# Optimization experiments

Hardware: AMD Instinct MI355X
Metric: run time of the kernel (lower is better)

Reference implementation:

```python
import jax, jax.numpy as jnp
import numpy as np

B, N, S, K, K2, C = 8, 131072, 1024, 64, 64, 32
RADIUS, RADIUS_POST = 0.4, 0.8
D1 = C + 6        # 38: mlp1 input (xyz + dim_box + feats)
H = 2 * C         # 64
D2 = H + 6        # 70: mlp2 input
H3 = 4 * H        # 256: mlp3 hidden


def _bgather(x, idx):
    # per-batch gather along axis 1 (points axis): x [B,N,...], idx [B,M] -> [B,M,...]
    return jax.vmap(lambda a, i: a[i])(x, idx)


def _conv_bn(x, w, s, t, relu=True):
    # 1x1 conv (matmul over channel) + folded eval-mode BN (scale/shift per channel)
    y = jnp.einsum('...c,cd->...d', x, w) * s + t
    return jnp.maximum(y, 0.0) if relu else y


def setup_inputs():
    key = jax.random.key(0)
    ks = jax.random.split(key, 20)
    inp = {
        'locs': jax.random.normal(ks[0], (B, N, 3), jnp.float32),
        'feats': jax.random.normal(ks[1], (B, C, N), jnp.float32),
        'boxes': jax.random.normal(ks[2], (B, N, 6), jnp.float32),
        'fps_inds': jax.random.randint(ks[3], (B, S), 0, N),
        'neighbor_inds': jax.random.randint(ks[4], (B, S * K), 0, N),
        'neighbor_inds2': jax.random.randint(ks[5], (B, S * K2), 0, S),
    }
    def w(k, i, o):
        return jax.random.normal(k, (i, o), jnp.float32) * (1.0 / np.sqrt(i))
    def bn(k, c):
        k1, k2 = jax.random.split(k)
        return (1.0 + 0.1 * jax.random.normal(k1, (c,), jnp.float32),
                0.1 * jax.random.normal(k2, (c,), jnp.float32))
    inp['w1a'] = w(ks[6], D1, C);  inp['s1a'], inp['t1a'] = bn(ks[7], C)
    inp['w1b'] = w(ks[8], C, H);   inp['s1b'], inp['t1b'] = bn(ks[9], H)
    inp['w2'] = w(ks[10], D2, H);  inp['s2'], inp['t2'] = bn(ks[11], H)
    inp['w3a'] = w(ks[12], H, H3); inp['s3a'], inp['t3a'] = bn(ks[13], H3)
    inp['w3b'] = w(ks[14], H3, H); inp['s3b'], inp['t3b'] = bn(ks[15], H)
    return inp


def reference(locs, feats, boxes, fps_inds, neighbor_inds, neighbor_inds2,
              w1a, s1a, t1a, w1b, s1b, t1b, w2, s2, t2,
              w3a, s3a, t3a, w3b, s3b, t3b):
    feats_nc = jnp.transpose(feats, (0, 2, 1))          # [B,N,C]
    dim_boxes = boxes[..., 3:] - boxes[..., :3]          # [B,N,3]

    fps_locs = _bgather(locs, fps_inds)                  # [B,S,3]
    fps_dim = _bgather(dim_boxes, fps_inds)              # [B,S,3]
    fps_boxes = _bgather(boxes, fps_inds)                # [B,S,6]

    # --- stage 1: ball-query gather on raw points ---
    gxyz = _bgather(locs, neighbor_inds).reshape(B, S, K, 3)
    gxyz = (gxyz - fps_locs[:, :, None, :]) / RADIUS
    gdim = _bgather(dim_boxes, neighbor_inds).reshape(B, S, K, 3)
    gdim = jnp.abs(gdim - fps_dim[:, :, None, :])
    gfeat = _bgather(feats_nc, neighbor_inds).reshape(B, S, K, C)
    g = jnp.concatenate([gxyz, gdim, gfeat], axis=-1)    # [B,S,K,38]

    h = _conv_bn(g, w1a, s1a, t1a, relu=True)
    h = _conv_bn(h, w1b, s1b, t1b, relu=True)            # [B,S,K,64]
    new_features = jnp.max(h, axis=2)                    # [B,S,64]
    identity = new_features

    # --- stage 2: ball-query gather on FPS points ---
    gxyz2 = _bgather(fps_locs, neighbor_inds2).reshape(B, S, K2, 3)
    gxyz2 = (gxyz2 - fps_locs[:, :, None, :]) / RADIUS_POST
    gdim2 = _bgather(fps_dim, neighbor_inds2).reshape(B, S, K2, 3)
    gdim2 = jnp.abs(gdim2 - fps_dim[:, :, None, :])
    gfeat2 = _bgather(new_features, neighbor_inds2).reshape(B, S, K2, H)
    g2 = jnp.concatenate([gxyz2, gdim2, gfeat2], axis=-1)  # [B,S,K2,70]

    h2 = _conv_bn(g2, w2, s2, t2, relu=False)            # [B,S,K2,64]
    h2 = jnp.max(h2, axis=2)                             # [B,S,64]

    # --- mlp_module3 (Conv1d bottleneck) + skip ---
    h3 = _conv_bn(h2, w3a, s3a, t3a, relu=True)          # [B,S,256]
    h3 = _conv_bn(h3, w3b, s3b, t3b, relu=False)         # [B,S,64]
    out = jnp.maximum(h3 + identity, 0.0)                # skip_act

    return fps_locs, jnp.transpose(out, (0, 2, 1)), fps_boxes, fps_inds
```

## Files before the change

### kernel.cpp

```cpp
#include <hip/hip_runtime.h>
#include <hip/hip_bf16.h>
#include <stdint.h>

#define DEV __device__ __forceinline__

constexpr int B_ = 8, N_ = 131072, S_ = 1024, C_ = 32;
constexpr float INV_R1 = 2.5f;
constexpr float INV_R2 = 1.25f;

constexpr int OW1AS = 0;
constexpr int OW1BS = 1216;
constexpr int OT1B  = 3264;
constexpr int OW2S  = 3328;
constexpr int OT2   = 7808;
constexpr int OW3AS = 7872;
constexpr int OT3A  = 24256;
constexpr int OW3BS = 24512;
constexpr int OT3B  = 40896;

constexpr size_t WS_CTR  = 163840;
constexpr size_t WS_NF   = WS_CTR  + (size_t)8192*104*4;
constexpr size_t WS_P2   = WS_NF   + (size_t)524288*4;
constexpr size_t WS_HOUT = WS_P2   + (size_t)524288*4;
constexpr size_t WS_PREC = WS_HOUT + (size_t)524288*4;

DEV float bfu(uint16_t u){ return __uint_as_float(((uint32_t)u) << 16); }

__global__ void k_weights(
    const float* __restrict__ w1a, const float* __restrict__ s1a,
    const float* __restrict__ w1b, const float* __restrict__ s1b,
    const float* __restrict__ t1b,
    const float* __restrict__ w2,  const float* __restrict__ s2,
    const float* __restrict__ t2,
    const float* __restrict__ w3a, const float* __restrict__ s3a,
    const float* __restrict__ t3a,
    const float* __restrict__ w3b, const float* __restrict__ s3b,
    const float* __restrict__ t3b,
    float* __restrict__ wsw)
{
  int t = blockIdx.x*256 + threadIdx.x;
  int nth = gridDim.x*256;
  for (int i=t;i<38*32;i+=nth)  wsw[OW1AS+i] = w1a[i]*s1a[i&31];
  for (int i=t;i<32*64;i+=nth)  wsw[OW1BS+i] = w1b[i]*s1b[i&63];
  for (int i=t;i<64;i+=nth)     wsw[OT1B+i]  = t1b[i];
  for (int i=t;i<70*64;i+=nth)  wsw[OW2S+i]  = w2[i]*s2[i&63];
  for (int i=t;i<64;i+=nth)     wsw[OT2+i]   = t2[i];
  for (int i=t;i<64*256;i+=nth) wsw[OW3AS+i] = w3a[i]*s3a[i&255];
  for (int i=t;i<256;i+=nth)    wsw[OT3A+i]  = t3a[i];
  for (int i=t;i<256*64;i+=nth) wsw[OW3BS+i] = w3b[i]*s3b[i&63];
  for (int i=t;i<64;i+=nth)     wsw[OT3B+i]  = t3b[i];
}

__global__ __launch_bounds__(256) void k_points(
    const float* __restrict__ locs,
    const float* __restrict__ feats,
    const float* __restrict__ wsw,
    __hip_bfloat16* __restrict__ prec)
{
  size_t p = (size_t)blockIdx.x*256 + threadIdx.x;
  int b = (int)(p >> 17);
  int pinb = (int)(p & (size_t)(N_-1));

  float x = locs[p*3+0]*INV_R1;
  float y = locs[p*3+1]*INV_R1;
  float z = locs[p*3+2]*INV_R1;

  float acc[32];
  #pragma unroll
  for (int j=0;j<32;j++)
    acc[j] = x*wsw[OW1AS+j] + y*wsw[OW1AS+32+j] + z*wsw[OW1AS+64+j];

  const float* fb = feats + (size_t)b*C_*N_ + pinb;
  float fcur[8], fnxt[8];
  #pragma unroll
  for (int i=0;i<8;i++) fcur[i] = fb[(size_t)i*N_];
  #pragma unroll
  for (int ch=0;ch<4;ch++){
    if (ch<3){
      #pragma unroll
      for (int i=0;i<8;i++) fnxt[i] = fb[(size_t)(8*(ch+1)+i)*N_];
    }
    #pragma unroll
    for (int i=0;i<8;i++){
      int c = 8*ch+i;
      #pragma unroll
      for (int j=0;j<32;j++)
        acc[j] = fmaf(fcur[i], wsw[OW1AS + (6+c)*32 + j], acc[j]);
    }
    #pragma unroll
    for (int i=0;i<8;i++) fcur[i] = fnxt[i];
  }
  union U { float4 v[4]; __hip_bfloat16 h[32]; } r;
  #pragma unroll
  for (int j=0;j<32;j++) r.h[j] = __float2bfloat16(acc[j]);
  float4* dst = (float4*)(prec + p*32);
  dst[0]=r.v[0]; dst[1]=r.v[1]; dst[2]=r.v[2]; dst[3]=r.v[3];
}

__global__ __launch_bounds__(256) void k_centers(
    const float* __restrict__ locs,
    const float* __restrict__ boxes,
    const int* __restrict__ fps_inds,
    const float* __restrict__ t1a,
    const float* __restrict__ wsw,
    float* __restrict__ ctr,
    float* __restrict__ out0,
    float* __restrict__ out2,
    float* __restrict__ out3)
{
  int i = blockIdx.x*256 + threadIdx.x;
  int b = i >> 10;
  int idx = fps_inds[i];
  size_t src = (size_t)b*N_ + (uint32_t)idx;

  float x = locs[src*3+0], y = locs[src*3+1], z = locs[src*3+2];
  out0[(size_t)i*3+0]=x; out0[(size_t)i*3+1]=y; out0[(size_t)i*3+2]=z;
  float bx0=boxes[src*6+0], bx1=boxes[src*6+1], bx2=boxes[src*6+2];
  float bx3=boxes[src*6+3], bx4=boxes[src*6+4], bx5=boxes[src*6+5];
  out2[(size_t)i*6+0]=bx0; out2[(size_t)i*6+1]=bx1; out2[(size_t)i*6+2]=bx2;
  out2[(size_t)i*6+3]=bx3; out2[(size_t)i*6+4]=bx4; out2[(size_t)i*6+5]=bx5;
  out3[i] = (float)idx;

  float d0=bx3-bx0, d1=bx4-bx1, d2=bx5-bx2;
  float* cr = ctr + (size_t)i*104;
  cr[0]=x; cr[1]=y; cr[2]=z; cr[3]=d0; cr[4]=d1; cr[5]=d2; cr[6]=0.f; cr[7]=0.f;
  float xr=x*INV_R1, yr=y*INV_R1, zr=z*INV_R1;
  #pragma unroll
  for (int j=0;j<32;j++)
    cr[8+j] = t1a[j] - xr*wsw[OW1AS+j] - yr*wsw[OW1AS+32+j] - zr*wsw[OW1AS+64+j];
  float xq=x*INV_R2, yq=y*INV_R2, zq=z*INV_R2;
  #pragma unroll
  for (int j=0;j<64;j++)
    cr[40+j] = wsw[OT2+j] - xq*wsw[OW2S+j] - yq*wsw[OW2S+64+j] - zq*wsw[OW2S+128+j];
}

__global__ __launch_bounds__(256) void k_stage1(
    const float* __restrict__ boxes,
    const int* __restrict__ neighbor_inds,
    const __hip_bfloat16* __restrict__ prec,
    const float* __restrict__ wsw,
    const float* __restrict__ ctr,
    float* __restrict__ nf,
    float* __restrict__ p2)
{
  int wid  = (blockIdx.x*256 + threadIdx.x) >> 6;
  int lane = threadIdx.x & 63;
  int uwid = __builtin_amdgcn_readfirstlane(wid);
  int b = uwid >> 10;

  int nbr = neighbor_inds[(size_t)uwid*64 + lane];
  size_t gp = (size_t)b*N_ + (uint32_t)nbr;

  union U { float4 v[4]; uint16_t u[32]; } r;
  const float4* psrc = (const float4*)(prec + gp*32);
  r.v[0]=psrc[0]; r.v[1]=psrc[1]; r.v[2]=psrc[2]; r.v[3]=psrc[3];

  const float2* bp = (const float2*)(boxes + gp*6);
  float2 q0=bp[0], q1=bp[1], q2=bp[2];

  const float* cr = ctr + (size_t)uwid*104;
  float ad0=fabsf((q1.y-q0.x)-cr[3]);
  float ad1=fabsf((q2.x-q0.y)-cr[4]);
  float ad2=fabsf((q2.y-q1.x)-cr[5]);

  float h[32];
  #pragma unroll
  for (int i=0;i<32;i++){
    float p = bfu(r.u[i]);
    float v = p + cr[8+i] + ad0*wsw[OW1AS+96+i] + ad1*wsw[OW1AS+128+i] + ad2*wsw[OW1AS+160+i];
    h[i] = fmaxf(v, 0.f);
  }
  float acc[64];
  #pragma unroll
  for (int j=0;j<64;j++) acc[j] = wsw[OT1B+j];
  #pragma unroll
  for (int i=0;i<32;i++){
    #pragma unroll
    for (int j=0;j<64;j++)
      acc[j] = fmaf(h[i], wsw[OW1BS + i*64 + j], acc[j]);
  }
  #pragma unroll
  for (int s=32;s>=1;s>>=1){
    bool up = (lane & s) != 0;
    #pragma unroll
    for (int i=0;i<s;i++){
      float lo = fmaxf(acc[i],   __shfl_xor(acc[i],   s));
      float hi = fmaxf(acc[s+i], __shfl_xor(acc[s+i], s));
      acc[i] = up ? hi : lo;
    }
  }
  float mine = fmaxf(acc[0], 0.f);
  nf[(size_t)uwid*64 + lane] = mine;

  float pv = (cr[0]*INV_R2)*wsw[OW2S+lane]
           + (cr[1]*INV_R2)*wsw[OW2S+64+lane]
           + (cr[2]*INV_R2)*wsw[OW2S+128+lane];
  #pragma unroll
  for (int i=0;i<64;i++)
    pv = fmaf(__shfl(mine, i), wsw[OW2S + (6+i)*64 + lane], pv);
  p2[(size_t)uwid*64 + lane] = pv;
}

__global__ __launch_bounds__(256) void k_stage23(
    const int* __restrict__ ninds2,
    const float* __restrict__ wsw,
    const float* __restrict__ ctr,
    const float* __restrict__ nf,
    const float* __restrict__ p2,
    float* __restrict__ hout)
{
  int wid  = (blockIdx.x*256 + threadIdx.x) >> 6;
  int lane = threadIdx.x & 63;
  int uw = __builtin_amdgcn_readfirstlane(wid);
  int c0 = uw*4;
  int bS = c0 & ~1023;

  float q2v[4], m[4], cd0[4], cd1[4], cd2[4];
  #pragma unroll
  for (int g=0;g<4;g++){
    const float* cr = ctr + (size_t)(c0+g)*104;
    q2v[g] = cr[40+lane];
    cd0[g]=cr[3]; cd1[g]=cr[4]; cd2[g]=cr[5];
    m[g] = -3.4e38f;
  }
  float w30 = wsw[OW2S+192+lane];
  float w31 = wsw[OW2S+256+lane];
  float w32 = wsw[OW2S+320+lane];

  #pragma unroll 4
  for (int k=0;k<64;k++){
    #pragma unroll
    for (int g=0;g<4;g++){
      int nb = ninds2[(size_t)(c0+g)*64 + k];
      int gg = bS + nb;
      const float* ncr = ctr + (size_t)gg*104;
      float a0 = fabsf(ncr[3]-cd0[g]);
      float a1 = fabsf(ncr[4]-cd1[g]);
      float a2 = fabsf(ncr[5]-cd2[g]);
      float v = p2[(size_t)gg*64 + lane] + q2v[g] + a0*w30 + a1*w31 + a2*w32;
      m[g] = fmaxf(m[g], v);
    }
  }

  float h3[4][4];
  #pragma unroll
  for (int g=0;g<4;g++)
    #pragma unroll
    for (int t=0;t<4;t++) h3[g][t] = wsw[OT3A + t*64 + lane];
  #pragma unroll 8
  for (int i=0;i<64;i++){
    float wv0 = wsw[OW3AS + i*256 +   0 + lane];
    float wv1 = wsw[OW3AS + i*256 +  64 + lane];
    float wv2 = wsw[OW3AS + i*256 + 128 + lane];
    float wv3 = wsw[OW3AS + i*256 + 192 + lane];
    #pragma unroll
    for (int g=0;g<4;g++){
      float h2i = __shfl(m[g], i);
      h3[g][0] = fmaf(h2i, wv0, h3[g][0]);
      h3[g][1] = fmaf(h2i, wv1, h3[g][1]);
      h3[g][2] = fmaf(h2i, wv2, h3[g][2]);
      h3[g][3] = fmaf(h2i, wv3, h3[g][3]);
    }
  }
  #pragma unroll
  for (int g=0;g<4;g++)
    #pragma unroll
    for (int t=0;t<4;t++) h3[g][t] = fmaxf(h3[g][t], 0.f);

  float o[4];
  #pragma unroll
  for (int g=0;g<4;g++) o[g] = wsw[OT3B + lane];
  #pragma unroll
  for (int t=0;t<4;t++){
    #pragma unroll 8
    for (int l=0;l<64;l++){
      float wb = wsw[OW3BS + (t*64+l)*64 + lane];
      #pragma unroll
      for (int g=0;g<4;g++)
        o[g] = fmaf(__shfl(h3[g][t], l), wb, o[g]);
    }
  }
  #pragma unroll
  for (int g=0;g<4;g++){
    float idv = nf[(size_t)(c0+g)*64 + lane];
    hout[(size_t)(c0+g)*64 + lane] = fmaxf(o[g] + idv, 0.f);
  }
}

__global__ __launch_bounds__(256) void k_transpose(
    const float* __restrict__ hout, float* __restrict__ out1)
{
  __shared__ float tile[64][65];
  int bb = blockIdx.x >> 4;
  int s0 = (blockIdx.x & 15) << 6;
  int c  = threadIdx.x & 63;
  int r4 = threadIdx.x >> 6;
  #pragma unroll
  for (int r=0;r<16;r++){
    int sr = r*4 + r4;
    tile[sr][c] = hout[((size_t)bb*S_ + s0 + sr)*64 + c];
  }
  __syncthreads();
  #pragma unroll
  for (int r=0;r<16;r++){
    int j = r*4 + r4;
    out1[(size_t)bb*64*S_ + (size_t)j*S_ + s0 + c] = tile[c][j];
  }
}

extern "C" void kernel_launch(void* const* d_in, const int* in_sizes, int n_in,
                              void* d_out, int out_size, void* d_ws, size_t ws_size,
                              hipStream_t stream) {
  const float* locs  = (const float*)d_in[0];
  const float* feats = (const float*)d_in[1];
  const float* boxes = (const float*)d_in[2];
  const int* fps_inds = (const int*)d_in[3];
  const int* ninds    = (const int*)d_in[4];
  const int* ninds2   = (const int*)d_in[5];
  const float* w1a=(const float*)d_in[6];
  const float* s1a=(const float*)d_in[7];
  const float* t1a=(const float*)d_in[8];
  const float* w1b=(const float*)d_in[9];
  const float* s1b=(const float*)d_in[10];
  const float* t1b=(const float*)d_in[11];
  const float* w2 =(const float*)d_in[12];
  const float* s2 =(const float*)d_in[13];
  const float* t2 =(const float*)d_in[14];
  const float* w3a=(const float*)d_in[15];
  const float* s3a=(const float*)d_in[16];
  const float* t3a=(const float*)d_in[17];
  const float* w3b=(const float*)d_in[18];
  const float* s3b=(const float*)d_in[19];
  const float* t3b=(const float*)d_in[20];

  float* wsw  = (float*)d_ws;
  float* ctr  = (float*)((char*)d_ws + WS_CTR);
  float* nf   = (float*)((char*)d_ws + WS_NF);
  float* p2b  = (float*)((char*)d_ws + WS_P2);
  float* hout = (float*)((char*)d_ws + WS_HOUT);
  __hip_bfloat16* prec = (__hip_bfloat16*)((char*)d_ws + WS_PREC);

  float* out  = (float*)d_out;
  float* out0 = out;
  float* out1 = out + 24576;
  float* out2 = out + 548864;
  float* out3 = out + 598016;

  k_weights<<<160, 256, 0, stream>>>(w1a,s1a,w1b,s1b,t1b,w2,s2,t2,w3a,s3a,t3a,w3b,s3b,t3b,wsw);
  k_points<<<4096, 256, 0, stream>>>(locs, feats, wsw, prec);
  k_centers<<<32, 256, 0, stream>>>(locs, boxes, fps_inds, t1a, wsw, ctr, out0, out2, out3);
  k_stage1<<<2048, 256, 0, stream>>>(boxes, ninds, prec, wsw, ctr, nf, p2b);
  k_stage23<<<512, 256, 0, stream>>>(ninds2, wsw, ctr, nf, p2b, hout);
  k_transpose<<<128, 256, 0, stream>>>(hout, out1);
}
```

Baseline: 401.6 us.

## Fuse center computation into stage1 and transpose into stage23 epilogue

Folds the per-FPS-center setup kernel into the stage-1 kernel, so each wave computes its own center terms and broadcasts them with shuffles instead of reading them back from the ctr buffer. It also drops the separate transpose kernel: stage23 now writes its four consecutive centers per channel straight into the channel-major output as a float4. This removes two launches and one intermediate round trip through global memory. The trade-off is strided float4 stores and some redundant per-wave center loads.

After: 398.2 us. No clear change (-0.8%).

```diff
diff --git a/kernel.cpp b/kernel.cpp
--- a/kernel.cpp
+++ b/kernel.cpp
@@ -97,117 +97,108 @@
   dst[0]=r.v[0]; dst[1]=r.v[1]; dst[2]=r.v[2]; dst[3]=r.v[3];
 }
 
-__global__ __launch_bounds__(256) void k_centers(
+__global__ __launch_bounds__(256) void k_stage1c(
     const float* __restrict__ locs,
     const float* __restrict__ boxes,
     const int* __restrict__ fps_inds,
     const float* __restrict__ t1a,
+    const int* __restrict__ ninds,
+    const __hip_bfloat16* __restrict__ prec,
     const float* __restrict__ wsw,
     float* __restrict__ ctr,
+    float* __restrict__ nf,
+    float* __restrict__ p2,
     float* __restrict__ out0,
     float* __restrict__ out2,
     float* __restrict__ out3)
-{
-  int i = blockIdx.x*256 + threadIdx.x;
-  int b = i >> 10;
-  int idx = fps_inds[i];
-  size_t src = (size_t)b*N_ + (uint32_t)idx;
-
-  float x = locs[src*3+0], y = locs[src*3+1], z = locs[src*3+2];
-  out0[(size_t)i*3+0]=x; out0[(size_t)i*3+1]=y; out0[(size_t)i*3+2]=z;
-  float bx0=boxes[src*6+0], bx1=boxes[src*6+1], bx2=boxes[src*6+2];
-  float bx3=boxes[src*6+3], bx4=boxes[src*6+4], bx5=boxes[src*6+5];
-  out2[(size_t)i*6+0]=bx0; out2[(size_t)i*6+1]=bx1; out2[(size_t)i*6+2]=bx2;
-  out2[(size_t)i*6+3]=bx3; out2[(size_t)i*6+4]=bx4; out2[(size_t)i*6+5]=bx5;
-  out3[i] = (float)idx;
-
-  float d0=bx3-bx0, d1=bx4-bx1, d2=bx5-bx2;
-  float* cr = ctr + (size_t)i*104;
-  cr[0]=x; cr[1]=y; cr[2]=z; cr[3]=d0; cr[4]=d1; cr[5]=d2; cr[6]=0.f; cr[7]=0.f;
-  float xr=x*INV_R1, yr=y*INV_R1, zr=z*INV_R1;
-  #pragma unroll
-  for (int j=0;j<32;j++)
-    cr[8+j] = t1a[j] - xr*wsw[OW1AS+j] - yr*wsw[OW1AS+32+j] - zr*wsw[OW1AS+64+j];
-  float xq=x*INV_R2, yq=y*INV_R2, zq=z*INV_R2;
-  #pragma unroll
-  for (int j=0;j<64;j++)
-    cr[40+j] = wsw[OT2+j] - xq*wsw[OW2S+j] - yq*wsw[OW2S+64+j] - zq*wsw[OW2S+128+j];
-}
-
-__global__ __launch_bounds__(256) void k_stage1(
-    const float* __restrict__ boxes,
-    const int* __restrict__ neighbor_inds,
-    const __hip_bfloat16* __restrict__ prec,
-    const float* __restrict__ wsw,
-    const float* __restrict__ ctr,
-    float* __restrict__ nf,
-    float* __restrict__ p2)
 {
   int wid  = (blockIdx.x*256 + threadIdx.x) >> 6;
   int lane = threadIdx.x & 63;
   int uwid = __builtin_amdgcn_readfirstlane(wid);
   int b = uwid >> 10;
 
-  int nbr = neighbor_inds[(size_t)uwid*64 + lane];
-  size_t gp = (size_t)b*N_ + (uint32_t)nbr;
-
-  union U { float4 v[4]; uint16_t u[32]; } r;
-  const float4* psrc = (const float4*)(prec + gp*32);
-  r.v[0]=psrc[0]; r.v[1]=psrc[1]; r.v[2]=psrc[2]; r.v[3]=psrc[3];
-
-  const float2* bp = (const float2*)(boxes + gp*6);
-  float2 q0=bp[0], q1=bp[1], q2=bp[2];
-
-  const float* cr = ctr + (size_t)uwid*104;
-  float ad0=fabsf((q1.y-q0.x)-cr[3]);
-  float ad1=fabsf((q2.x-q0.y)-cr[4]);
-  float ad2=fabsf((q2.y-q1.x)-cr[5]);
-
-  float h[32];
-  #pragma unroll
-  for (int i=0;i<32;i++){
-    float p = bfu(r.u[i]);
-    float v = p + cr[8+i] + ad0*wsw[OW1AS+96+i] + ad1*wsw[OW1AS+128+i] + ad2*wsw[OW1AS+160+i];
-    h[i] = fmaxf(v, 0.f);
-  }
-  float acc[64];
-  #pragma unroll
-  for (int j=0;j<64;j++) acc[j] = wsw[OT1B+j];
-  #pragma unroll
-  for (int i=0;i<32;i++){
-    #pragma unroll
-    for (int j=0;j<64;j++)
-      acc[j] = fmaf(h[i], wsw[OW1BS + i*64 + j], acc[j]);
-  }
-  #pragma unroll
-  for (int s=32;s>=1;s>>=1){
-    bool up = (lane & s) != 0;
-    #pragma unroll
-    for (int i=0;i<s;i++){
-      float lo = fmaxf(acc[i],   __shfl_xor(acc[i],   s));
-      float hi = fmaxf(acc[s+i], __shfl_xor(acc[s+i], s));
-      acc[i] = up ? hi : lo;
-    }
-  }
-  float mine = fmaxf(acc[0], 0.f);
-  nf[(size_t)uwid*64 + lane] = mine;
-
-  float pv = (cr[0]*INV_R2)*wsw[OW2S+lane]
-           + (cr[1]*INV_R2)*wsw[OW2S+64+lane]
-           + (cr[2]*INV_R2)*wsw[OW2S+128+lane];
-  #pragma unroll
-  for (int i=0;i<64;i++)
-    pv = fmaf(__shfl(mine, i), wsw[OW2S + (6+i)*64 + lane], pv);
-  p2[(size_t)uwid*64 + lane] = pv;
-}
-
-__global__ __launch_bounds__(256) void k_stage23(
+  int idx = fps_inds[uwid];
+  size_t src = (size_t)b*N_ + (uint32_t)idx;
+  float cx = locs[src*3+0], cy = locs[src*3+1], cz = locs[src*3+2];
+  float bx0=boxes[src*6+0], bx1=boxes[src*6+1], bx2=boxes[src*6+2];
+  float bx3=boxes[src*6+3], bx4=boxes[src*6+4], bx5=boxes[src*6+5];
+  float d0=bx3-bx0, d1=bx4-bx1, d2=bx5-bx2;
+
+  if (lane==0){
+    out0[(size_t)uwid*3+0]=cx; out0[(size_t)uwid*3+1]=cy; out0[(size_t)uwid*3+2]=cz;
+    out2[(size_t)uwid*6+0]=bx0; out2[(size_t)uwid*6+1]=bx1; out2[(size_t)uwid*6+2]=bx2;
+    out2[(size_t)uwid*6+3]=bx3; out2[(size_t)uwid*6+4]=bx4; out2[(size_t)uwid*6+5]=bx5;
+    out3[uwid] = (float)idx;
+    ctr[(size_t)uwid*104+3]=d0; ctr[(size_t)uwid*104+4]=d1; ctr[(size_t)uwid*104+5]=d2;
+  }
+  {
+    int j = lane & 31;
+    float xr=cx*INV_R1, yr=cy*INV_R1, zr=cz*INV_R1;
+    float c8 = t1a[j] - xr*wsw[OW1AS+j] - yr*wsw[OW1AS+32+j] - zr*wsw[OW1AS+64+j];
+    float xq=cx*INV_R2, yq=cy*INV_R2, zq=cz*INV_R2;
+    float q2l = wsw[OT2+lane] - xq*wsw[OW2S+lane] - yq*wsw[OW2S+64+lane] - zq*wsw[OW2S+128+lane];
+    ctr[(size_t)uwid*104+40+lane] = q2l;
+
+    int nbr = ninds[(size_t)uwid*64 + lane];
+    size_t gp = (size_t)b*N_ + (uint32_t)nbr;
+
+    union U { float4 v[4]; uint16_t u[32]; } r;
+    const float4* psrc = (const float4*)(prec + gp*32);
+    r.v[0]=psrc[0]; r.v[1]=psrc[1]; r.v[2]=psrc[2]; r.v[3]=psrc[3];
+
+    const float2* bp = (const float2*)(boxes + gp*6);
+    float2 q0=bp[0], q1=bp[1], q2=bp[2];
+
+    float ad0=fabsf((q1.y-q0.x)-d0);
+    float ad1=fabsf((q2.x-q0.y)-d1);
+    float ad2=fabsf((q2.y-q1.x)-d2);
+
+    float h[32];
+    #pragma unroll
+    for (int i=0;i<32;i++){
+      float p = bfu(r.u[i]);
+      float v = p + __shfl(c8, i) + ad0*wsw[OW1AS+96+i] + ad1*wsw[OW1AS+128+i] + ad2*wsw[OW1AS+160+i];
+      h[i] = fmaxf(v, 0.f);
+    }
+    float acc[64];
+    #pragma unroll
+    for (int j2=0;j2<64;j2++) acc[j2] = wsw[OT1B+j2];
+    #pragma unroll
+    for (int i=0;i<32;i++){
+      #pragma unroll
+      for (int j2=0;j2<64;j2++)
+        acc[j2] = fmaf(h[i], wsw[OW1BS + i*64 + j2], acc[j2]);
+    }
+    #pragma unroll
+    for (int s=32;s>=1;s>>=1){
+      bool up = (lane & s) != 0;
+      #pragma unroll
+      for (int i=0;i<s;i++){
+        float lo = fmaxf(acc[i],   __shfl_xor(acc[i],   s));
+        float hi = fmaxf(acc[s+i], __shfl_xor(acc[s+i], s));
+        acc[i] = up ? hi : lo;
+      }
+    }
+    float mine = fmaxf(acc[0], 0.f);
+    nf[(size_t)uwid*64 + lane] = mine;
+
+    float pv = (cx*INV_R2)*wsw[OW2S+lane]
+             + (cy*INV_R2)*wsw[OW2S+64+lane]
+             + (cz*INV_R2)*wsw[OW2S+128+lane];
+    #pragma unroll
+    for (int i=0;i<64;i++)
+      pv = fmaf(__shfl(mine, i), wsw[OW2S + (6+i)*64 + lane], pv);
+    p2[(size_t)uwid*64 + lane] = pv;
+  }
+}
+
+__global__ __launch_bounds__(256) void k_stage23t(
     const int* __restrict__ ninds2,
     const float* __restrict__ wsw,
     const float* __restrict__ ctr,
     const float* __restrict__ nf,
     const float* __restrict__ p2,
-    float* __restrict__ hout)
+    float* __restrict__ out1)
 {
   int wid  = (blockIdx.x*256 + threadIdx.x) >> 6;
   int lane = threadIdx.x & 63;
@@ -280,32 +271,17 @@
         o[g] = fmaf(__shfl(h3[g][t], l), wb, o[g]);
     }
   }
+  float4 vals;
+  float* vp = &vals.x;
   #pragma unroll
   for (int g=0;g<4;g++){
     float idv = nf[(size_t)(c0+g)*64 + lane];
-    hout[(size_t)(c0+g)*64 + lane] = fmaxf(o[g] + idv, 0.f);
-  }
-}
-
-__global__ __launch_bounds__(256) void k_transpose(
-    const float* __restrict__ hout, float* __restrict__ out1)
-{
-  __shared__ float tile[64][65];
-  int bb = blockIdx.x >> 4;
-  int s0 = (blockIdx.x & 15) << 6;
-  int c  = threadIdx.x & 63;
-  int r4 = threadIdx.x >> 6;
-  #pragma unroll
-  for (int r=0;r<16;r++){
-    int sr = r*4 + r4;
-    tile[sr][c] = hout[((size_t)bb*S_ + s0 + sr)*64 + c];
-  }
-  __syncthreads();
-  #pragma unroll
-  for (int r=0;r<16;r++){
-    int j = r*4 + r4;
-    out1[(size_t)bb*64*S_ + (size_t)j*S_ + s0 + c] = tile[c][j];
-  }
+    vp[g] = fmaxf(o[g] + idv, 0.f);
+  }
+  int b = c0 >> 10;
+  int s = c0 & 1023;
+  float4* dst = (float4*)(out1 + ((size_t)b*64 + lane)*S_ + s);
+  *dst = vals;
 }
 
 extern "C" void kernel_launch(void* const* d_in, const int* in_sizes, int n_in,
@@ -337,7 +313,6 @@
   float* ctr  = (float*)((char*)d_ws + WS_CTR);
   float* nf   = (float*)((char*)d_ws + WS_NF);
   float* p2b  = (float*)((char*)d_ws + WS_P2);
-  float* hout = (float*)((char*)d_ws + WS_HOUT);
   __hip_bfloat16* prec = (__hip_bfloat16*)((char*)d_ws + WS_PREC);
 
   float* out  = (float*)d_out;
@@ -348,8 +323,6 @@
 
   k_weights<<<160, 256, 0, stream>>>(w1a,s1a,w1b,s1b,t1b,w2,s2,t2,w3a,s3a,t3a,w3b,s3b,t3b,wsw);
   k_points<<<4096, 256, 0, stream>>>(locs, feats, wsw, prec);
-  k_centers<<<32, 256, 0, stream>>>(locs, boxes, fps_inds, t1a, wsw, ctr, out0, out2, out3);
-  k_stage1<<<2048, 256, 0, stream>>>(boxes, ninds, prec, wsw, ctr, nf, p2b);
-  k_stage23<<<512, 256, 0, stream>>>(ninds2, wsw, ctr, nf, p2b, hout);
-  k_transpose<<<128, 256, 0, stream>>>(hout, out1);
-}
+  k_stage1c<<<2048, 256, 0, stream>>>(locs, boxes, fps_inds, t1a, ninds, prec, wsw, ctr, nf, p2b, out0, out2, out3);
+  k_stage23t<<<512, 256, 0, stream>>>(ninds2, wsw, ctr, nf, p2b, out1);
+}
```
